# Kernel tuning notes

Hardware: AMD Instinct MI355X
Metric: run time of the kernel (lower is better)

Reference implementation:

```python
import jax, jax.numpy as jnp
import numpy as np

NEG_SLOPE = 0.2  # PyG GATConv default


def add_self_loops(edge_index, num_nodes):
    loops = jnp.arange(num_nodes, dtype=edge_index.dtype)
    return jnp.concatenate([edge_index, jnp.stack([loops, loops])], axis=1)


def gat_conv(x, edge_index, W, att_src, att_dst, bias, heads, out_ch, concat):
    # x: [N, F_in]; edge_index: [2, E] with row0=src(j), row1=dst(i)
    N = x.shape[0]
    xl = (x @ W).reshape(N, heads, out_ch)              # [N, H, C]
    src, dst = edge_index[0], edge_index[1]
    a_src = jnp.einsum('nhc,hc->nh', xl, att_src)        # [N, H]
    a_dst = jnp.einsum('nhc,hc->nh', xl, att_dst)        # [N, H]
    alpha = jax.nn.leaky_relu(a_src[src] + a_dst[dst], NEG_SLOPE)  # [E, H]
    # segment softmax over incoming edges of each dst node
    m = jax.ops.segment_max(alpha, dst, num_segments=N)  # [N, H]
    e = jnp.exp(alpha - m[dst])
    denom = jax.ops.segment_sum(e, dst, num_segments=N)
    coef = e / (denom[dst] + 1e-16)                      # [E, H]
    msg = xl[src] * coef[..., None]                      # [E, H, C]
    out = jax.ops.segment_sum(msg, dst, num_segments=N)  # [N, H, C]
    out = out.reshape(N, heads * out_ch) if concat else out.mean(axis=1)
    return out + bias


def setup_inputs() -> dict:
    key = jax.random.key(0)
    ks = jax.random.split(key, 12)
    N, E = 50000, 800000
    nfeat, nhid, nheads, nclass = 512, 8, 8, 16
    hid = nhid * nheads  # 64
    s1 = 1.0 / np.sqrt(nfeat)
    s2 = 1.0 / np.sqrt(hid)
    return {
        'x': jax.random.normal(ks[0], (N, nfeat), jnp.float32),
        'edge_index': jax.random.randint(ks[1], (2, E), 0, N, jnp.int64 if jax.config.jax_enable_x64 else jnp.int32),
        'W1': jax.random.uniform(ks[2], (nfeat, hid), jnp.float32, -s1, s1),
        'att_src1': jax.random.uniform(ks[3], (nheads, nhid), jnp.float32, -s2, s2),
        'att_dst1': jax.random.uniform(ks[4], (nheads, nhid), jnp.float32, -s2, s2),
        'bias1': jnp.zeros((hid,), jnp.float32),
        'W2': jax.random.uniform(ks[5], (hid, nclass), jnp.float32, -s2, s2),
        'att_src2': jax.random.uniform(ks[6], (1, nclass), jnp.float32, -0.25, 0.25),
        'att_dst2': jax.random.uniform(ks[7], (1, nclass), jnp.float32, -0.25, 0.25),
        'bias2': jnp.zeros((nclass,), jnp.float32),
    }


def reference(x, edge_index, W1, att_src1, att_dst1, bias1, W2, att_src2, att_dst2, bias2):
    N = x.shape[0]
    ei = add_self_loops(edge_index, N)
    # dropout layers are identity at inference
    h = gat_conv(x, ei, W1, att_src1, att_dst1, bias1, heads=8, out_ch=8, concat=True)
    o = gat_conv(h, ei, W2, att_src2, att_dst2, bias2, heads=1, out_ch=16, concat=True)
    o = jax.nn.elu(o)
    return jax.nn.log_softmax(o, axis=1)
```

## Files before the change

### kernel.cpp

```cpp
#include <hip/hip_runtime.h>
#include <math.h>

#define NEG_SLOPE 0.2f

typedef short short8 __attribute__((ext_vector_type(8)));
typedef float floatx4 __attribute__((ext_vector_type(4)));

static __device__ __forceinline__ float bf2f(unsigned short u) {
  return __uint_as_float(((unsigned int)u) << 16);
}
static __device__ __forceinline__ unsigned short f2bf(float f) {
  unsigned int u = __float_as_uint(f);
  u = (u + 0x7fffu + ((u >> 16) & 1u)) >> 16;
  return (unsigned short)u;
}
static __device__ __forceinline__ unsigned int pack2(float a, float b) {
  return (unsigned int)f2bf(a) | ((unsigned int)f2bf(b) << 16);
}

__global__ void init_misc(const float* __restrict__ W1, unsigned short* __restrict__ W1t,
                          int* __restrict__ deg, int N) {
  int b = blockIdx.x;
  if (b < 128) {
    int i = b * 256 + threadIdx.x;
    int k = i >> 6, c = i & 63;
    W1t[c * 512 + k] = f2bf(W1[i]);
  } else {
    int n = (b - 128) * 256 + threadIdx.x;
    if (n < N) deg[n] = 1;
  }
}

__global__ __launch_bounds__(256) void gemm1_hist(const float* __restrict__ A,
                                                  const unsigned short* __restrict__ W1t,
                                                  const float* __restrict__ att_src,
                                                  const float* __restrict__ att_dst,
                                                  unsigned short* __restrict__ xlb,
                                                  float* __restrict__ a_src,
                                                  float* __restrict__ a_dst, int M,
                                                  const int* __restrict__ ei,
                                                  int* __restrict__ deg, int E,
                                                  int ipc, int G1) {
  __shared__ unsigned short As[64 * 72];
  __shared__ unsigned short Bs[64 * 72];
  if ((int)blockIdx.x >= G1) {
    int b = blockIdx.x - G1;
    int slice = b & 7;
    int chunk = b >> 3;
    int lo = (int)(((long long)slice * M) >> 3);
    int hi = (int)(((long long)(slice + 1) * M) >> 3);
    int beg = chunk * ipc;
    int end = min(beg + ipc, E);
    for (int i = beg + threadIdx.x; i < end; i += 256) {
      int d = ei[E + i];
      if (d >= lo && d < hi) atomicAdd(&deg[d], 1);
    }
    return;
  }
  int tid = threadIdx.x;
  int w = tid >> 6, lane = tid & 63;
  int q = lane >> 4, cl = lane & 15;
  int row0 = blockIdx.x << 6;
  floatx4 acc[4] = {};

  int sr = tid >> 2;
  int skq = (tid & 3) << 4;
  int arow = row0 + sr;
  bool okA = arow < M;
  const float* Aptr = A + (size_t)arow * 512 + skq;
  const unsigned short* Bptr = W1t + sr * 512 + skq;
  unsigned short* AsW = As + sr * 72 + skq;
  unsigned short* BsW = Bs + sr * 72 + skq;

  float4 ca0 = make_float4(0.f, 0.f, 0.f, 0.f), ca1 = ca0, ca2 = ca0, ca3 = ca0;
  uint4 cb0, cb1;
  if (okA) {
    ca0 = *(const float4*)(Aptr);
    ca1 = *(const float4*)(Aptr + 4);
    ca2 = *(const float4*)(Aptr + 8);
    ca3 = *(const float4*)(Aptr + 12);
  }
  cb0 = *(const uint4*)(Bptr);
  cb1 = *(const uint4*)(Bptr + 8);

#pragma unroll
  for (int k0 = 0; k0 < 512; k0 += 64) {
    __syncthreads();
    uint4 a0, a1;
    a0.x = pack2(ca0.x, ca0.y); a0.y = pack2(ca0.z, ca0.w);
    a0.z = pack2(ca1.x, ca1.y); a0.w = pack2(ca1.z, ca1.w);
    a1.x = pack2(ca2.x, ca2.y); a1.y = pack2(ca2.z, ca2.w);
    a1.z = pack2(ca3.x, ca3.y); a1.w = pack2(ca3.z, ca3.w);
    *(uint4*)(AsW) = a0;
    *(uint4*)(AsW + 8) = a1;
    *(uint4*)(BsW) = cb0;
    *(uint4*)(BsW + 8) = cb1;
    __syncthreads();
    if (k0 < 448) {
      ca0 = make_float4(0.f, 0.f, 0.f, 0.f); ca1 = ca0; ca2 = ca0; ca3 = ca0;
      if (okA) {
        ca0 = *(const float4*)(Aptr + k0 + 64);
        ca1 = *(const float4*)(Aptr + k0 + 68);
        ca2 = *(const float4*)(Aptr + k0 + 72);
        ca3 = *(const float4*)(Aptr + k0 + 76);
      }
      cb0 = *(const uint4*)(Bptr + k0 + 64);
      cb1 = *(const uint4*)(Bptr + k0 + 72);
    }
#pragma unroll
    for (int kk = 0; kk < 2; ++kk) {
      short8 af = *(const short8*)(As + (w * 16 + cl) * 72 + kk * 32 + q * 8);
#pragma unroll
      for (int t = 0; t < 4; ++t) {
        short8 bf = *(const short8*)(Bs + (t * 16 + cl) * 72 + kk * 32 + q * 8);
        acc[t] = __builtin_amdgcn_mfma_f32_16x16x32_bf16(af, bf, acc[t], 0, 0, 0);
      }
    }
  }

  float asv[4], adv[4];
#pragma unroll
  for (int t = 0; t < 4; ++t) {
    asv[t] = att_src[t * 16 + cl];
    adv[t] = att_dst[t * 16 + cl];
  }
#pragma unroll
  for (int reg = 0; reg < 4; ++reg) {
    int r = row0 + w * 16 + q * 4 + reg;
    bool ok = r < M;
#pragma unroll
    for (int t = 0; t < 4; ++t) {
      float v = acc[t][reg];
      if (ok) xlb[(size_t)r * 64 + t * 16 + cl] = f2bf(v);
      float ps = v * asv[t];
      float pd = v * adv[t];
      ps += __shfl_xor(ps, 1); pd += __shfl_xor(pd, 1);
      ps += __shfl_xor(ps, 2); pd += __shfl_xor(pd, 2);
      ps += __shfl_xor(ps, 4); pd += __shfl_xor(pd, 4);
      if (ok && (cl & 7) == 0) {
        int h = t * 2 + (cl >> 3);
        a_src[r * 8 + h] = ps;
        a_dst[r * 8 + h] = pd;
      }
    }
  }
}

__global__ __launch_bounds__(1024) void scan_single(const int* __restrict__ deg,
                                                    int* __restrict__ rowptr,
                                                    int* __restrict__ cursor, int N) {
  __shared__ int wsum[16];
  int tid = threadIdx.x;
  int lane = tid & 63, wv = tid >> 6;
  int carry = 0;
  for (int base = 0; base < N; base += 8192) {
    int i0 = base + tid * 8;
    int d[8];
    if (i0 + 8 <= N) {
      int4 a = *(const int4*)(deg + i0);
      int4 b = *(const int4*)(deg + i0 + 4);
      d[0] = a.x; d[1] = a.y; d[2] = a.z; d[3] = a.w;
      d[4] = b.x; d[5] = b.y; d[6] = b.z; d[7] = b.w;
    } else {
#pragma unroll
      for (int k = 0; k < 8; ++k) d[k] = (i0 + k < N) ? deg[i0 + k] : 0;
    }
    int e[8];
    e[0] = d[0];
#pragma unroll
    for (int k = 1; k < 8; ++k) e[k] = e[k - 1] + d[k];
    int tot = e[7];
    int v = tot;
#pragma unroll
    for (int off = 1; off < 64; off <<= 1) {
      int t = __shfl_up(v, off, 64);
      if (lane >= off) v += t;
    }
    if (lane == 63) wsum[wv] = v;
    __syncthreads();
    int woff = carry;
    for (int w = 0; w < wv; ++w) woff += wsum[w];
    int excl = woff + v - tot;
    int r[8];
    r[0] = excl;
#pragma unroll
    for (int k = 1; k < 8; ++k) r[k] = excl + e[k - 1];
    if (i0 + 8 <= N) {
      *(int4*)(rowptr + i0)     = make_int4(r[0], r[1], r[2], r[3]);
      *(int4*)(rowptr + i0 + 4) = make_int4(r[4], r[5], r[6], r[7]);
      *(int4*)(cursor + i0)     = make_int4(r[0], r[1], r[2], r[3]);
      *(int4*)(cursor + i0 + 4) = make_int4(r[4], r[5], r[6], r[7]);
    } else {
#pragma unroll
      for (int k = 0; k < 8; ++k)
        if (i0 + k < N) { rowptr[i0 + k] = r[k]; cursor[i0 + k] = r[k]; }
    }
    int bt = 0;
#pragma unroll
    for (int w = 0; w < 16; ++w) bt += wsum[w];
    carry += bt;
    __syncthreads();
  }
  if (tid == 0) rowptr[N] = carry;
}

__global__ __launch_bounds__(256) void scatter_sliced(const int* __restrict__ ei,
                                                      int* __restrict__ cursor,
                                                      int* __restrict__ srcs,
                                                      int E, int N, int ipc) {
  int slice = blockIdx.x & 7;
  int chunk = blockIdx.x >> 3;
  int lo = (int)(((long long)slice * N) >> 3);
  int hi = (int)(((long long)(slice + 1) * N) >> 3);
  int total = E + N;
  int beg = chunk * ipc;
  int end = min(beg + ipc, total);
  for (int i = beg + threadIdx.x; i < end; i += 256) {
    int d = (i < E) ? ei[E + i] : (i - E);
    if (d >= lo && d < hi) {
      int s = (i < E) ? ei[i] : d;
      int pos = atomicAdd(&cursor[d], 1);
      srcs[pos] = s;
    }
  }
}

__global__ __launch_bounds__(256) void agg1_fused(const int* __restrict__ rowptr,
                                                  const int* __restrict__ srcs,
                                                  const float* __restrict__ a_src,
                                                  const float* __restrict__ a_dst,
                                                  const unsigned short* __restrict__ xlb,
                                                  const float* __restrict__ bias1,
                                                  const float* __restrict__ W2,
                                                  const float* __restrict__ att_src2,
                                                  const float* __restrict__ att_dst2,
                                                  float* __restrict__ xl2,
                                                  float* __restrict__ a_src2,
                                                  float* __restrict__ a_dst2, int N) {
  __shared__ float W2s[64 * 16];
  __shared__ float hsm[4][64];
  int tid = threadIdx.x;
  W2s[tid]       = W2[tid];
  W2s[tid + 256] = W2[tid + 256];
  W2s[tid + 512] = W2[tid + 512];
  W2s[tid + 768] = W2[tid + 768];
  __syncthreads();

  int wv = tid >> 6, lane = tid & 63;
  int node = (blockIdx.x << 2) + wv;
  if (node >= N) return;
  int half = lane >> 5;
  int j = lane & 31;
  int h = j >> 2;
  int beg = rowptr[node], end = rowptr[node + 1];
  float ad = a_dst[node * 8 + h];
  float den = 0.f, acc0 = 0.f, acc1 = 0.f;

  int p = beg + half;
  bool v0 = p < end, v1 = p + 2 < end, v2 = p + 4 < end, v3 = p + 6 < end;
  int s0 = srcs[v0 ? p : beg];
  int s1 = srcs[v1 ? p + 2 : beg];
  int s2 = srcs[v2 ? p + 4 : beg];
  int s3 = srcs[v3 ? p + 6 : beg];
  while (v0) {
    int np = p + 8;
    bool u0 = np < end, u1 = np + 2 < end, u2 = np + 4 < end, u3 = np + 6 < end;
    int t0 = srcs[u0 ? np : beg];
    int t1 = srcs[u1 ? np + 2 : beg];
    int t2 = srcs[u2 ? np + 4 : beg];
    int t3 = srcs[u3 ? np + 6 : beg];
    float a0 = a_src[s0 * 8 + h] + ad;
    float a1 = a_src[s1 * 8 + h] + ad;
    float a2 = a_src[s2 * 8 + h] + ad;
    float a3 = a_src[s3 * 8 + h] + ad;
    ushort2 x0 = *(const ushort2*)(xlb + (size_t)s0 * 64 + 2 * j);
    ushort2 x1 = *(const ushort2*)(xlb + (size_t)s1 * 64 + 2 * j);
    ushort2 x2 = *(const ushort2*)(xlb + (size_t)s2 * 64 + 2 * j);
    ushort2 x3 = *(const ushort2*)(xlb + (size_t)s3 * 64 + 2 * j);
    a0 = a0 >= 0.f ? a0 : NEG_SLOPE * a0;
    a1 = a1 >= 0.f ? a1 : NEG_SLOPE * a1;
    a2 = a2 >= 0.f ? a2 : NEG_SLOPE * a2;
    a3 = a3 >= 0.f ? a3 : NEG_SLOPE * a3;
    float w0 = v0 ? __expf(a0) : 0.f;
    float w1 = v1 ? __expf(a1) : 0.f;
    float w2 = v2 ? __expf(a2) : 0.f;
    float w3 = v3 ? __expf(a3) : 0.f;
    den += (w0 + w1) + (w2 + w3);
    acc0 += w0 * bf2f(x0.x) + w1 * bf2f(x1.x) + w2 * bf2f(x2.x) + w3 * bf2f(x3.x);
    acc1 += w0 * bf2f(x0.y) + w1 * bf2f(x1.y) + w2 * bf2f(x2.y) + w3 * bf2f(x3.y);
    p = np;
    s0 = t0; s1 = t1; s2 = t2; s3 = t3;
    v0 = u0; v1 = u1; v2 = u2; v3 = u3;
  }
  den  += __shfl_xor(den, 32);
  acc0 += __shfl_xor(acc0, 32);
  acc1 += __shfl_xor(acc1, 32);
  float inv = 1.f / (den + 1e-16f);
  float2 bv = *(const float2*)(bias1 + 2 * j);
  float h0 = acc0 * inv + bv.x;
  float h1 = acc1 * inv + bv.y;
  if (half == 0) {
    hsm[wv][2 * j]     = h0;
    hsm[wv][2 * j + 1] = h1;
  }
  if (lane < 16) {
    float sum = 0.f;
#pragma unroll
    for (int k = 0; k < 64; ++k) sum += hsm[wv][k] * W2s[k * 16 + lane];
    xl2[(size_t)node * 16 + lane] = sum;
    float ps = sum * att_src2[lane];
    float pd = sum * att_dst2[lane];
#pragma unroll
    for (int w = 8; w >= 1; w >>= 1) {
      ps += __shfl_xor(ps, w, 16);
      pd += __shfl_xor(pd, w, 16);
    }
    if (lane == 0) { a_src2[node] = ps; a_dst2[node] = pd; }
  }
}

__global__ __launch_bounds__(256) void agg2_fin(const int* __restrict__ rowptr,
                                                const int* __restrict__ srcs,
                                                const float* __restrict__ a_src2,
                                                const float* __restrict__ a_dst2,
                                                const float* __restrict__ xl2,
                                                const float* __restrict__ bias2,
                                                float* __restrict__ out, int N) {
  int t = blockIdx.x * blockDim.x + threadIdx.x;
  int node = t >> 4;
  int c = t & 15;
  if (node >= N) return;
  int beg = rowptr[node], end = rowptr[node + 1];
  float ad = a_dst2[node];
  float den = 0.f, acc = 0.f;
  int p = beg;
  bool v0 = true, v1 = p + 1 < end, v2 = p + 2 < end, v3 = p + 3 < end;
  int s0 = srcs[p];
  int s1 = srcs[v1 ? p + 1 : beg];
  int s2 = srcs[v2 ? p + 2 : beg];
  int s3 = srcs[v3 ? p + 3 : beg];
  while (v0) {
    int np = p + 4;
    bool u0 = np < end, u1 = np + 1 < end, u2 = np + 2 < end, u3 = np + 3 < end;
    int t0 = srcs[u0 ? np : beg];
    int t1 = srcs[u1 ? np + 1 : beg];
    int t2 = srcs[u2 ? np + 2 : beg];
    int t3 = srcs[u3 ? np + 3 : beg];
    float a0 = a_src2[s0] + ad, a1 = a_src2[s1] + ad;
    float a2 = a_src2[s2] + ad, a3 = a_src2[s3] + ad;
    float x0 = xl2[(size_t)s0 * 16 + c], x1 = xl2[(size_t)s1 * 16 + c];
    float x2 = xl2[(size_t)s2 * 16 + c], x3 = xl2[(size_t)s3 * 16 + c];
    a0 = a0 >= 0.f ? a0 : NEG_SLOPE * a0;
    a1 = a1 >= 0.f ? a1 : NEG_SLOPE * a1;
    a2 = a2 >= 0.f ? a2 : NEG_SLOPE * a2;
    a3 = a3 >= 0.f ? a3 : NEG_SLOPE * a3;
    float w0 = v0 ? __expf(a0) : 0.f;
    float w1 = v1 ? __expf(a1) : 0.f;
    float w2 = v2 ? __expf(a2) : 0.f;
    float w3 = v3 ? __expf(a3) : 0.f;
    den += (w0 + w1) + (w2 + w3);
    acc += w0 * x0 + w1 * x1 + w2 * x2 + w3 * x3;
    p = np;
    s0 = t0; s1 = t1; s2 = t2; s3 = t3;
    v0 = u0; v1 = u1; v2 = u2; v3 = u3;
  }
  float o = acc / (den + 1e-16f) + bias2[c];
  o = o > 0.f ? o : expm1f(o);
  float mx = o;
#pragma unroll
  for (int w = 8; w >= 1; w >>= 1) mx = fmaxf(mx, __shfl_xor(mx, w, 16));
  float e = __expf(o - mx);
  float ssum = e;
#pragma unroll
  for (int w = 8; w >= 1; w >>= 1) ssum += __shfl_xor(ssum, w, 16);
  out[(size_t)node * 16 + c] = o - mx - logf(ssum);
}

static inline size_t rnd16(size_t x) { return (x + 15) & ~(size_t)15; }

extern "C" void kernel_launch(void* const* d_in, const int* in_sizes, int n_in,
                              void* d_out, int out_size, void* d_ws, size_t ws_size,
                              hipStream_t stream) {
  const float* x        = (const float*)d_in[0];
  const int*   ei       = (const int*)d_in[1];
  const float* W1       = (const float*)d_in[2];
  const float* att_src1 = (const float*)d_in[3];
  const float* att_dst1 = (const float*)d_in[4];
  const float* bias1    = (const float*)d_in[5];
  const float* W2       = (const float*)d_in[6];
  const float* att_src2 = (const float*)d_in[7];
  const float* att_dst2 = (const float*)d_in[8];
  const float* bias2    = (const float*)d_in[9];
  float* out = (float*)d_out;

  int N = in_sizes[0] / 512;
  int E = in_sizes[1] / 2;

  char* ws = (char*)d_ws;
  unsigned short* xlb = (unsigned short*)ws;  ws += rnd16((size_t)N * 64 * 2);
  unsigned short* W1t = (unsigned short*)ws;  ws += rnd16((size_t)512 * 64 * 2);
  float* a_src1 = (float*)ws;                 ws += rnd16((size_t)N * 8 * 4);
  float* a_dst1 = (float*)ws;                 ws += rnd16((size_t)N * 8 * 4);
  float* xl2    = (float*)ws;                 ws += rnd16((size_t)N * 16 * 4);
  float* a_src2 = (float*)ws;                 ws += rnd16((size_t)N * 4);
  float* a_dst2 = (float*)ws;                 ws += rnd16((size_t)N * 4);
  int* deg      = (int*)ws;                   ws += rnd16((size_t)N * 4);
  int* rowptr   = (int*)ws;                   ws += rnd16((size_t)(N + 1) * 4);
  int* cursor   = (int*)ws;                   ws += rnd16((size_t)N * 4);
  int* srcs     = (int*)ws;                   ws += rnd16((size_t)(E + N) * 4);

  const int NCHUNK = 256;
  int G1 = (N + 63) / 64;
  int ipc_h = (E + NCHUNK - 1) / NCHUNK;
  int ipc_s = (E + N + NCHUNK - 1) / NCHUNK;

  init_misc<<<128 + (N + 255) / 256, 256, 0, stream>>>(W1, W1t, deg, N);
  gemm1_hist<<<G1 + NCHUNK * 8, 256, 0, stream>>>(x, W1t, att_src1, att_dst1,
                                                  xlb, a_src1, a_dst1, N,
                                                  ei, deg, E, ipc_h, G1);
  scan_single<<<1, 1024, 0, stream>>>(deg, rowptr, cursor, N);
  scatter_sliced<<<NCHUNK * 8, 256, 0, stream>>>(ei, cursor, srcs, E, N, ipc_s);
  agg1_fused<<<(N + 3) / 4, 256, 0, stream>>>(rowptr, srcs, a_src1, a_dst1, xlb,
                                              bias1, W2, att_src2, att_dst2,
                                              xl2, a_src2, a_dst2, N);
  agg2_fin<<<((size_t)N * 16 + 255) / 256, 256, 0, stream>>>(rowptr, srcs, a_src2, a_dst2,
                                                             xl2, bias2, out, N);
}
```

Baseline: 311.5 us.

## Load GEMM1 MFMA fragments directly from global memory, dropping LDS staging

The first-layer GEMM no longer stages A and W1t tiles through shared memory with double syncthreads per k-step. Each wave now loads its MFMA A and B fragments straight from global memory (B from the small W1t, which should stay in cache) and converts A to bf16 in registers. This removes LDS traffic and barriers and lowers LDS usage, which may raise occupancy. In exchange there is no software prefetch, so each thread issues 32-byte strided loads per row, and coalescing and latency hiding depend on the compiler's unrolling.

```diff
diff --git a/kernel.cpp b/kernel.cpp
--- a/kernel.cpp
+++ b/kernel.cpp
@@ -41,8 +41,6 @@
                                                   const int* __restrict__ ei,
                                                   int* __restrict__ deg, int E,
                                                   int ipc, int G1) {
-  __shared__ unsigned short As[64 * 72];
-  __shared__ unsigned short Bs[64 * 72];
   if ((int)blockIdx.x >= G1) {
     int b = blockIdx.x - G1;
     int slice = b & 7;
@@ -61,60 +59,26 @@
   int w = tid >> 6, lane = tid & 63;
   int q = lane >> 4, cl = lane & 15;
   int row0 = blockIdx.x << 6;
+  int ar = row0 + w * 16 + cl;
+  int arc = ar < M ? ar : 0;
+  const float* Ap = A + (size_t)arc * 512 + q * 8;
+  const unsigned short* Bp = W1t + cl * 512 + q * 8;
   floatx4 acc[4] = {};
 
-  int sr = tid >> 2;
-  int skq = (tid & 3) << 4;
-  int arow = row0 + sr;
-  bool okA = arow < M;
-  const float* Aptr = A + (size_t)arow * 512 + skq;
-  const unsigned short* Bptr = W1t + sr * 512 + skq;
-  unsigned short* AsW = As + sr * 72 + skq;
-  unsigned short* BsW = Bs + sr * 72 + skq;
-
-  float4 ca0 = make_float4(0.f, 0.f, 0.f, 0.f), ca1 = ca0, ca2 = ca0, ca3 = ca0;
-  uint4 cb0, cb1;
-  if (okA) {
-    ca0 = *(const float4*)(Aptr);
-    ca1 = *(const float4*)(Aptr + 4);
-    ca2 = *(const float4*)(Aptr + 8);
-    ca3 = *(const float4*)(Aptr + 12);
-  }
-  cb0 = *(const uint4*)(Bptr);
-  cb1 = *(const uint4*)(Bptr + 8);
-
-#pragma unroll
-  for (int k0 = 0; k0 < 512; k0 += 64) {
-    __syncthreads();
-    uint4 a0, a1;
-    a0.x = pack2(ca0.x, ca0.y); a0.y = pack2(ca0.z, ca0.w);
-    a0.z = pack2(ca1.x, ca1.y); a0.w = pack2(ca1.z, ca1.w);
-    a1.x = pack2(ca2.x, ca2.y); a1.y = pack2(ca2.z, ca2.w);
-    a1.z = pack2(ca3.x, ca3.y); a1.w = pack2(ca3.z, ca3.w);
-    *(uint4*)(AsW) = a0;
-    *(uint4*)(AsW + 8) = a1;
-    *(uint4*)(BsW) = cb0;
-    *(uint4*)(BsW + 8) = cb1;
-    __syncthreads();
-    if (k0 < 448) {
-      ca0 = make_float4(0.f, 0.f, 0.f, 0.f); ca1 = ca0; ca2 = ca0; ca3 = ca0;
-      if (okA) {
-        ca0 = *(const float4*)(Aptr + k0 + 64);
-        ca1 = *(const float4*)(Aptr + k0 + 68);
-        ca2 = *(const float4*)(Aptr + k0 + 72);
-        ca3 = *(const float4*)(Aptr + k0 + 76);
-      }
-      cb0 = *(const uint4*)(Bptr + k0 + 64);
-      cb1 = *(const uint4*)(Bptr + k0 + 72);
-    }
-#pragma unroll
-    for (int kk = 0; kk < 2; ++kk) {
-      short8 af = *(const short8*)(As + (w * 16 + cl) * 72 + kk * 32 + q * 8);
-#pragma unroll
-      for (int t = 0; t < 4; ++t) {
-        short8 bf = *(const short8*)(Bs + (t * 16 + cl) * 72 + kk * 32 + q * 8);
-        acc[t] = __builtin_amdgcn_mfma_f32_16x16x32_bf16(af, bf, acc[t], 0, 0, 0);
-      }
+#pragma unroll
+  for (int ks = 0; ks < 16; ++ks) {
+    int k0 = ks * 32;
+    float4 fa = *(const float4*)(Ap + k0);
+    float4 fb = *(const float4*)(Ap + k0 + 4);
+    union { uint4 u; short8 s; } cva;
+    cva.u.x = pack2(fa.x, fa.y);
+    cva.u.y = pack2(fa.z, fa.w);
+    cva.u.z = pack2(fb.x, fb.y);
+    cva.u.w = pack2(fb.z, fb.w);
+#pragma unroll
+    for (int t = 0; t < 4; ++t) {
+      short8 bf = *(const short8*)(Bp + t * 16 * 512 + k0);
+      acc[t] = __builtin_amdgcn_mfma_f32_16x16x32_bf16(cva.s, bf, acc[t], 0, 0, 0);
     }
   }
 
```

Measured after the change: 320.4 us. +2.9%, slower.
